# Kernel optimization log

Hardware: AMD Instinct MI355X
Metric: run time of the kernel (lower is better)

Reference implementation:

```python
import jax, jax.numpy as jnp
import numpy as np

N_NODES = 50000
N_EDGES = 300000
N_GRAPHS = 256
F_IN = 78
H1 = 10
F_H1 = 78
F_OUT = 128
NEG_SLOPE = 0.2  # PyG GATConv default leaky_relu slope


def gat_conv(x, src, dst, W, a_src, a_dst, bias, heads, out_dim):
    """PyG GATConv (eval mode): linear -> per-edge attention -> segment softmax over
    destination nodes -> scatter-add aggregation -> concat heads + bias.
    src/dst already include self-loops."""
    N = x.shape[0]
    h = (x @ W).reshape(N, heads, out_dim)              # [N,H,F]
    al_s = (h * a_src[None]).sum(-1)                     # [N,H]
    al_d = (h * a_dst[None]).sum(-1)                     # [N,H]
    e = jax.nn.leaky_relu(al_s[src] + al_d[dst], NEG_SLOPE)  # [E,H]
    m = jax.ops.segment_max(e, dst, num_segments=N)      # stable softmax per dst node
    w = jnp.exp(e - m[dst])
    denom = jax.ops.segment_sum(w, dst, num_segments=N)
    alpha = w / denom[dst]                               # [E,H]
    out = jax.ops.segment_sum(h[src] * alpha[:, :, None], dst, num_segments=N)
    return out.reshape(N, heads * out_dim) + bias


def setup_inputs() -> dict:
    key = jax.random.key(0)
    ks = jax.random.split(key, 16)
    x = jax.random.normal(ks[0], (N_NODES, F_IN), dtype=jnp.float32)
    edge_index = jax.random.randint(ks[1], (2, N_EDGES), 0, N_NODES, dtype=jnp.int32)
    batch = jnp.sort(jax.random.randint(ks[2], (N_NODES,), 0, N_GRAPHS, dtype=jnp.int32))
    s = 0.1
    W1 = jax.random.normal(ks[3], (F_IN, H1 * F_H1), dtype=jnp.float32) * s
    a_src1 = jax.random.normal(ks[4], (H1, F_H1), dtype=jnp.float32) * s
    a_dst1 = jax.random.normal(ks[5], (H1, F_H1), dtype=jnp.float32) * s
    b1 = jnp.zeros((H1 * F_H1,), dtype=jnp.float32)
    W2 = jax.random.normal(ks[6], (H1 * F_H1, F_OUT), dtype=jnp.float32) * s
    a_src2 = jax.random.normal(ks[7], (1, F_OUT), dtype=jnp.float32) * s
    a_dst2 = jax.random.normal(ks[8], (1, F_OUT), dtype=jnp.float32) * s
    b2 = jnp.zeros((F_OUT,), dtype=jnp.float32)
    fc_w = jax.random.normal(ks[9], (F_OUT, F_OUT), dtype=jnp.float32) * s
    fc_b = jnp.zeros((F_OUT,), dtype=jnp.float32)
    return dict(x=x, edge_index=edge_index, batch=batch, W1=W1, a_src1=a_src1,
                a_dst1=a_dst1, b1=b1, W2=W2, a_src2=a_src2, a_dst2=a_dst2, b2=b2,
                fc_w=fc_w, fc_b=fc_b)


def reference(x, edge_index, batch, W1, a_src1, a_dst1, b1, W2, a_src2, a_dst2, b2, fc_w, fc_b):
    N = x.shape[0]
    loop = jnp.arange(N, dtype=edge_index.dtype)
    src = jnp.concatenate([edge_index[0], loop])  # add self-loops (PyG default)
    dst = jnp.concatenate([edge_index[1], loop])
    # dropout layers are identity in eval mode
    h = jax.nn.elu(gat_conv(x, src, dst, W1, a_src1, a_dst1, b1, H1, F_H1))
    h = gat_conv(h, src, dst, W2, a_src2, a_dst2, b2, 1, F_OUT)
    h = jax.nn.relu(h)
    g = jax.ops.segment_max(h, batch, num_segments=N_GRAPHS)  # global max pool [B,F]
    out = jax.nn.relu(g @ fc_w + fc_b)
    return out
```

## Files before the change

### kernel.cpp

```cpp
#include <hip/hip_runtime.h>
#include <hip/hip_bf16.h>

#define N_NODES 50000
#define N_EDGES 300000
#define E_TOT   350000
#define N_GRAPHS 256
#define F_IN 78
#define H1 10
#define D1 780
#define F_OUT 128
#define KP 800
#define K1P 96
#define NEG_SLOPE 0.2f
#define NB 196

typedef float v4f __attribute__((ext_vector_type(4)));
typedef short v8s __attribute__((ext_vector_type(8)));

__device__ __forceinline__ int src_of(int e, const int* __restrict__ ei) {
  return (e < N_EDGES) ? ei[e] : (e - N_EDGES);
}
__device__ __forceinline__ int dst_of(int e, const int* __restrict__ ei) {
  return (e < N_EDGES) ? ei[N_EDGES + e] : (e - N_EDGES);
}


__global__ void k_deg(const int* __restrict__ ei, int* __restrict__ deg) {
  int e = blockIdx.x * 256 + threadIdx.x;
  if (e >= E_TOT) return;
  atomicAdd(&deg[dst_of(e, ei)], 1);
}

__global__ void k_scan1(const int* __restrict__ deg, int* __restrict__ part) {
  __shared__ int s[256];
  int t = threadIdx.x;
  int i = blockIdx.x * 256 + t;
  s[t] = (i < N_NODES) ? deg[i] : 0;
  __syncthreads();
  for (int d = 128; d > 0; d >>= 1) {
    if (t < d) s[t] += s[t + d];
    __syncthreads();
  }
  if (t == 0) part[blockIdx.x] = s[0];
}

__global__ void k_scan2(const int* __restrict__ part, int* __restrict__ ppref) {
  if (threadIdx.x == 0) {
    int run = 0;
    for (int i = 0; i < NB; ++i) { ppref[i] = run; run += part[i]; }
  }
}

__global__ void k_scan3(const int* __restrict__ deg, const int* __restrict__ ppref,
                        int* __restrict__ offs, int* __restrict__ cursor) {
  __shared__ int s[256];
  int t = threadIdx.x;
  int i = blockIdx.x * 256 + t;
  int v = (i < N_NODES) ? deg[i] : 0;
  s[t] = v;
  __syncthreads();
  for (int d = 1; d < 256; d <<= 1) {
    int u = (t >= d) ? s[t - d] : 0;
    __syncthreads();
    s[t] += u;
    __syncthreads();
  }
  int excl = s[t] - v;
  if (i < N_NODES) {
    int off = ppref[blockIdx.x] + excl;
    offs[i] = off;
    cursor[i] = off;
  }
}

__global__ void k_scatter(const int* __restrict__ ei, int* __restrict__ cursor,
                          int* __restrict__ src_s, int* __restrict__ dst_s) {
  int e = blockIdx.x * 256 + threadIdx.x;
  if (e >= E_TOT) return;
  int s = src_of(e, ei);
  int d = dst_of(e, ei);
  int pos = atomicAdd(&cursor[d], 1);
  src_s[pos] = s;
  dst_s[pos] = d;
}


__global__ void k_prep(const float* __restrict__ W1, const float* __restrict__ as1,
                       const float* __restrict__ ad1, float* __restrict__ was,
                       float* __restrict__ wad) {
  int i = blockIdx.x * 256 + threadIdx.x;
  if (i >= F_IN * H1) return;
  int k = i / H1, h = i - k * H1;
  const float* wrow = W1 + (size_t)k * D1 + h * 78;
  const float* ar = as1 + h * 78;
  const float* br = ad1 + h * 78;
  float s = 0.f, d = 0.f;
  for (int f = 0; f < 78; ++f) {
    float w = wrow[f];
    s = fmaf(w, ar[f], s);
    d = fmaf(w, br[f], d);
  }
  was[i] = s;
  wad[i] = d;
}


__global__ __launch_bounds__(320) void k_logits1(const float* __restrict__ x,
                                                 const float* __restrict__ was,
                                                 const float* __restrict__ wad,
                                                 float* __restrict__ als,
                                                 float* __restrict__ ald) {
  __shared__ float xs[32][81];
  __shared__ float wl[D1], wl2[D1];
  int tid = threadIdx.x;
  int n0 = blockIdx.x * 32;
  for (int i = tid; i < 32 * F_IN; i += 320) {
    int r = i / F_IN, k = i - r * F_IN;
    int n = n0 + r;
    xs[r][k] = (n < N_NODES) ? x[(size_t)n * F_IN + k] : 0.f;
  }
  for (int i = tid; i < D1; i += 320) { wl[i] = was[i]; wl2[i] = wad[i]; }
  __syncthreads();
  int r = tid / 10, h = tid - r * 10;
  int n = n0 + r;
  float s = 0.f, d = 0.f;
  for (int k = 0; k < F_IN; ++k) {
    float xv = xs[r][k];
    s = fmaf(xv, wl[k * 10 + h], s);
    d = fmaf(xv, wl2[k * 10 + h], d);
  }
  if (n < N_NODES) { als[n * 10 + h] = s; ald[n * 10 + h] = d; }
}


__global__ void k_w1e(const float* __restrict__ als1, const float* __restrict__ ald1,
                      const int* __restrict__ src_s, const int* __restrict__ dst_s,
                      float* __restrict__ w1) {
  int i = blockIdx.x * 256 + threadIdx.x;
  if (i >= E_TOT * H1) return;
  int pos = i / H1, h = i - pos * H1;
  float v = als1[src_s[pos] * H1 + h] + ald1[dst_s[pos] * H1 + h];
  v = (v > 0.f) ? v : NEG_SLOPE * v;
  w1[i] = __expf(v);
}


__global__ void k_w1t(const float* __restrict__ W1, __hip_bfloat16* __restrict__ T) {
  int i = blockIdx.x * 256 + threadIdx.x;
  if (i >= 800 * K1P) return;
  int r = i / K1P, k = i - r * K1P;
  float v = (r < D1 && k < F_IN) ? W1[(size_t)k * D1 + r] : 0.f;
  T[i] = __float2bfloat16(v);
}


__global__ void k_w2t(const float* __restrict__ W2, __hip_bfloat16* __restrict__ Bt) {
  int i = blockIdx.x * 256 + threadIdx.x;
  if (i >= F_OUT * KP) return;
  int c = i / KP, k = i - c * KP;
  float v = (k < D1) ? W2[(size_t)k * F_OUT + c] : 0.f;
  Bt[i] = __float2bfloat16(v);
}


__global__ __launch_bounds__(512, 4) void k_l12(const float* __restrict__ x,
                                                const float* __restrict__ w1,
                                                const int* __restrict__ src_s,
                                                const int* __restrict__ offs,
                                                const int* __restrict__ deg,
                                                const __hip_bfloat16* __restrict__ W1T,
                                                const float* __restrict__ b1,
                                                const __hip_bfloat16* __restrict__ W2T,
                                                const float* __restrict__ a_src2,
                                                const float* __restrict__ a_dst2,
                                                float* __restrict__ h2,
                                                float* __restrict__ als2,
                                                float* __restrict__ ald2) {
  __shared__ __align__(16) unsigned char lds[33792];
  __hip_bfloat16* xbb = (__hip_bfloat16*)lds;
  __hip_bfloat16* out1t = (__hip_bfloat16*)lds;
  float* h2t = (float*)(lds + 25600);
#define XB(h, g, k) xbb[((h) * 16 + (g)) * 104 + (k)]

  int tid = threadIdx.x, wid = tid >> 6, lane = tid & 63;
  int n0 = blockIdx.x * 16;
  int col16 = lane & 15, kq = (lane >> 4) * 8;

  {
    unsigned int* p = (unsigned int*)lds;
    for (int i = tid; i < H1 * 16 * 52; i += 512) p[i] = 0u;
  }
  __syncthreads();

  #pragma unroll
  for (int rep = 0; rep < 2; ++rep) {
    int g = wid * 2 + rep;
    int n = n0 + g;
    int o = __builtin_amdgcn_readfirstlane(offs[n]);
    int d = __builtin_amdgcn_readfirstlane(deg[n]);
    float acc[H1], acc2[H1];
    #pragma unroll
    for (int h = 0; h < H1; ++h) { acc[h] = 0.f; acc2[h] = 0.f; }

    float onesel = (lane == 14) ? 1.0f : 0.f;
    int j = 0;
    for (; j + 4 <= d; j += 4) {
      int e0 = o + j;
      int s0 = src_s[e0], s1 = src_s[e0 + 1], s2 = src_s[e0 + 2], s3 = src_s[e0 + 3];
      const float* x0 = x + (size_t)s0 * F_IN;
      const float* x1 = x + (size_t)s1 * F_IN;
      const float* x2 = x + (size_t)s2 * F_IN;
      const float* x3 = x + (size_t)s3 * F_IN;
      float xa0 = x0[lane], xa1 = x1[lane], xa2 = x2[lane], xa3 = x3[lane];
      float xb0 = (lane < 14) ? x0[64 + lane] : onesel;
      float xb1 = (lane < 14) ? x1[64 + lane] : onesel;
      float xb2 = (lane < 14) ? x2[64 + lane] : onesel;
      float xb3 = (lane < 14) ? x3[64 + lane] : onesel;
      const float* wp = w1 + (size_t)e0 * H1;
      #pragma unroll
      for (int h = 0; h < H1; ++h) {
        float wa = wp[h], wb = wp[10 + h], wc = wp[20 + h], wd = wp[30 + h];
        acc[h] = fmaf(wa, xa0, acc[h]);
        acc[h] = fmaf(wb, xa1, acc[h]);
        acc[h] = fmaf(wc, xa2, acc[h]);
        acc[h] = fmaf(wd, xa3, acc[h]);
        acc2[h] = fmaf(wa, xb0, acc2[h]);
        acc2[h] = fmaf(wb, xb1, acc2[h]);
        acc2[h] = fmaf(wc, xb2, acc2[h]);
        acc2[h] = fmaf(wd, xb3, acc2[h]);
      }
    }
    for (; j < d; ++j) {
      int e0 = o + j;
      int s0 = src_s[e0];
      const float* x0 = x + (size_t)s0 * F_IN;
      float xa0 = x0[lane];
      float xb0 = (lane < 14) ? x0[64 + lane] : onesel;
      const float* wp = w1 + (size_t)e0 * H1;
      #pragma unroll
      for (int h = 0; h < H1; ++h) {
        float wa = wp[h];
        acc[h] = fmaf(wa, xa0, acc[h]);
        acc2[h] = fmaf(wa, xb0, acc2[h]);
      }
    }
    #pragma unroll
    for (int h = 0; h < H1; ++h) {
      float inv = 1.f / __shfl(acc2[h], 14);
      XB(h, g, lane) = __float2bfloat16(acc[h] * inv);
      if (lane < 14) XB(h, g, 64 + lane) = __float2bfloat16(acc2[h] * inv);
    }
  }
  __syncthreads();

  const unsigned short* Bp1 = (const unsigned short*)W1T;
  v4f res[7];
  int nu = 0;
  for (int u = wid; u < 50; u += 8) {
    int h = u / 5, nt = u - (u / 5) * 5;
    v4f acc = (v4f){0.f, 0.f, 0.f, 0.f};
    #pragma unroll
    for (int kt = 0; kt < 3; ++kt) {
      v8s a = *reinterpret_cast<const v8s*>(&XB(h, col16, kt * 32 + kq));
      v8s b = *reinterpret_cast<const v8s*>(
          &Bp1[(size_t)(h * 78 + nt * 16 + col16) * K1P + kt * 32 + kq]);
      acc = __builtin_amdgcn_mfma_f32_16x16x32_bf16(a, b, acc, 0, 0, 0);
    }
    res[nu++] = acc;
  }
  __syncthreads();

  if (tid < 160) {
    int node = tid / 10, cc = (tid - node * 10) * 2;
    *(unsigned int*)&out1t[node * 800 + 780 + cc] = 0u;
  }
  nu = 0;
  for (int u = wid; u < 50; u += 8) {
    int h = u / 5, nt = u - (u / 5) * 5;
    v4f acc = res[nu++];
    int cl = nt * 16 + col16;
    if (cl < 78) {
      int c = h * 78 + cl;
      float bv = b1[c];
      #pragma unroll
      for (int r = 0; r < 4; ++r) {
        int node = (lane >> 4) * 4 + r;
        float v = acc[r] + bv;
        v = (v > 0.f) ? v : expm1f(v);
        out1t[node * 800 + c] = __float2bfloat16(v);
      }
    }
  }
  __syncthreads();

  const unsigned short* Bp2 = (const unsigned short*)W2T;
  v4f acc3 = (v4f){0.f, 0.f, 0.f, 0.f};
  #pragma unroll 5
  for (int kt = 0; kt < 25; ++kt) {
    int k = kt * 32 + kq;
    v8s a = *reinterpret_cast<const v8s*>(&out1t[col16 * 800 + k]);
    v8s b = *reinterpret_cast<const v8s*>(&Bp2[(size_t)(wid * 16 + col16) * KP + k]);
    acc3 = __builtin_amdgcn_mfma_f32_16x16x32_bf16(a, b, acc3, 0, 0, 0);
  }
  {
    int col = wid * 16 + col16;
    #pragma unroll
    for (int r = 0; r < 4; ++r) {
      int node = (lane >> 4) * 4 + r;
      h2[(size_t)(n0 + node) * F_OUT + col] = acc3[r];
      h2t[node * F_OUT + col] = acc3[r];
    }
  }
  __syncthreads();

  #pragma unroll
  for (int rep = 0; rep < 2; ++rep) {
    int nn = wid * 2 + rep;
    float v0 = h2t[nn * F_OUT + lane], v1 = h2t[nn * F_OUT + 64 + lane];
    float s = v0 * a_src2[lane] + v1 * a_src2[64 + lane];
    float dd = v0 * a_dst2[lane] + v1 * a_dst2[64 + lane];
    #pragma unroll
    for (int off = 32; off > 0; off >>= 1) {
      s += __shfl_down(s, off);
      dd += __shfl_down(dd, off);
    }
    if (lane == 0) { als2[n0 + nn] = s; ald2[n0 + nn] = dd; }
  }
#undef XB
}


__global__ __launch_bounds__(512) void k_agg2f(const float* __restrict__ h2,
                                               const float* __restrict__ als2,
                                               const float* __restrict__ ald2,
                                               const int* __restrict__ src_s,
                                               const int* __restrict__ offs,
                                               const int* __restrict__ deg,
                                               const float* __restrict__ b2,
                                               const int* __restrict__ batch,
                                               unsigned int* __restrict__ g) {
  int tid = threadIdx.x;
  int n = blockIdx.x * 4 + (tid >> 7);
  int f = tid & 127;
  int o = __builtin_amdgcn_readfirstlane(offs[n]);
  int d = __builtin_amdgcn_readfirstlane(deg[n]);
  float aldn = ald2[n];
  float acc = 0.f, ssum = 0.f;
  int j = 0;
  for (; j + 4 <= d; j += 4) {
    float wq[4], hq[4];
    #pragma unroll
    for (int q = 0; q < 4; ++q) {
      int e = o + j + q;
      int sb = src_s[e];
      float v = als2[sb] + aldn;
      v = (v > 0.f) ? v : NEG_SLOPE * v;
      wq[q] = __expf(v);
      hq[q] = h2[(size_t)sb * F_OUT + f];
    }
    #pragma unroll
    for (int q = 0; q < 4; ++q) {
      ssum += wq[q];
      acc = fmaf(wq[q], hq[q], acc);
    }
  }
  for (; j < d; ++j) {
    int e = o + j;
    int sb = src_s[e];
    float v = als2[sb] + aldn;
    v = (v > 0.f) ? v : NEG_SLOPE * v;
    float w = __expf(v);
    ssum += w;
    acc = fmaf(w, h2[(size_t)sb * F_OUT + f], acc);
  }
  float v = fmaxf(acc / ssum + b2[f], 0.f);
  int gc = __builtin_amdgcn_readfirstlane(batch[n]);
  atomicMax(&g[gc * F_OUT + f], __float_as_uint(v));
}


__global__ __launch_bounds__(128) void k_fc(const float* __restrict__ g,
                                            const float* __restrict__ fc_w,
                                            const float* __restrict__ fc_b,
                                            float* __restrict__ out) {
  int b = blockIdx.x, c = threadIdx.x;
  const float* gr = g + (size_t)b * F_OUT;
  float acc = 0.f;
  for (int k = 0; k < F_OUT; ++k) acc = fmaf(gr[k], fc_w[k * F_OUT + c], acc);
  float v = acc + fc_b[c];
  out[(size_t)b * F_OUT + c] = fmaxf(v, 0.f);
}


extern "C" void kernel_launch(void* const* d_in, const int* in_sizes, int n_in,
                              void* d_out, int out_size, void* d_ws, size_t ws_size,
                              hipStream_t stream) {
  const float* x      = (const float*)d_in[0];
  const int*   ei     = (const int*)  d_in[1];
  const int*   batch  = (const int*)  d_in[2];
  const float* W1     = (const float*)d_in[3];
  const float* a_src1 = (const float*)d_in[4];
  const float* a_dst1 = (const float*)d_in[5];
  const float* b1     = (const float*)d_in[6];
  const float* W2     = (const float*)d_in[7];
  const float* a_src2 = (const float*)d_in[8];
  const float* a_dst2 = (const float*)d_in[9];
  const float* b2     = (const float*)d_in[10];
  const float* fc_w   = (const float*)d_in[11];
  const float* fc_b   = (const float*)d_in[12];
  float* out = (float*)d_out;

  float* ws = (float*)d_ws;
  float* h2   = ws;
  float* als1 = ws + 6400000;
  float* ald1 = ws + 6900000;
  float* als2 = ws + 7400000;
  float* ald2 = ws + 7450000;
  float* g    = ws + 7500000;
  float* was  = ws + 7533000;
  float* wad  = ws + 7534000;
  __hip_bfloat16* W2T = (__hip_bfloat16*)(ws + 7535000);
  __hip_bfloat16* W1T = (__hip_bfloat16*)(ws + 7587000);
  float* w1   = ws + 7626000;
  int* ib     = (int*)(ws + 11126000);
  int* deg    = ib;
  int* offs   = ib + 50000;
  int* cursor = ib + 100000;
  int* src_s  = ib + 150000;
  int* dst_s  = ib + 500000;
  int* part   = ib + 850000;
  int* ppref  = ib + 850224;

  hipMemsetAsync(deg, 0, N_NODES * sizeof(int), stream);
  k_deg<<<(E_TOT + 255) / 256, 256, 0, stream>>>(ei, deg);
  k_scan1<<<NB, 256, 0, stream>>>(deg, part);
  k_scan2<<<1, 64, 0, stream>>>(part, ppref);
  k_scan3<<<NB, 256, 0, stream>>>(deg, ppref, offs, cursor);
  k_scatter<<<(E_TOT + 255) / 256, 256, 0, stream>>>(ei, cursor, src_s, dst_s);

  k_prep<<<4, 256, 0, stream>>>(W1, a_src1, a_dst1, was, wad);
  k_w1t<<<(800 * K1P + 255) / 256, 256, 0, stream>>>(W1, W1T);
  k_w2t<<<(F_OUT * KP + 255) / 256, 256, 0, stream>>>(W2, W2T);
  hipMemsetAsync(g, 0, N_GRAPHS * F_OUT * sizeof(float), stream);

  k_logits1<<<(N_NODES + 31) / 32, 320, 0, stream>>>(x, was, wad, als1, ald1);
  k_w1e<<<(E_TOT * H1 + 255) / 256, 256, 0, stream>>>(als1, ald1, src_s, dst_s, w1);

  k_l12<<<N_NODES / 16, 512, 0, stream>>>(x, w1, src_s, offs, deg, W1T, b1,
                                          W2T, a_src2, a_dst2, h2, als2, ald2);

  k_agg2f<<<(N_NODES + 3) / 4, 512, 0, stream>>>(h2, als2, ald2, src_s, offs, deg,
                                                 b2, batch, (unsigned int*)g);

  k_fc<<<N_GRAPHS, F_OUT, 0, stream>>>(g, fc_w, fc_b, out);
}
```

Before: 267.1 us.

## Sort nodes by degree to balance per-wave work in aggregation kernels

Adds a counting sort of nodes by in-degree (histogram, scan, scatter kernels) and makes the fused layer kernel and the layer-2 aggregation process nodes in that order through an indirection array. Waves in a block then handle nodes of similar degree, which is meant to reduce divergence and idle time from uneven neighbour counts. In exchange it adds three small kernels, an extra indirection load, scattered writes of h2 and logits, and less locality in reads of per-node data.

```diff
diff --git a/kernel.cpp b/kernel.cpp
--- a/kernel.cpp
+++ b/kernel.cpp
@@ -82,6 +82,28 @@
   int pos = atomicAdd(&cursor[d], 1);
   src_s[pos] = s;
   dst_s[pos] = d;
+}
+
+
+__global__ void k_dhist(const int* __restrict__ deg, int* __restrict__ hist) {
+  int n = blockIdx.x * 256 + threadIdx.x;
+  if (n >= N_NODES) return;
+  atomicAdd(&hist[min(deg[n], 63)], 1);
+}
+
+__global__ void k_dscan(const int* __restrict__ hist, int* __restrict__ bincur) {
+  if (threadIdx.x == 0) {
+    int run = 0;
+    for (int i = 0; i < 64; ++i) { bincur[i] = run; run += hist[i]; }
+  }
+}
+
+__global__ void k_dscatter(const int* __restrict__ deg, int* __restrict__ bincur,
+                           int* __restrict__ nsort) {
+  int n = blockIdx.x * 256 + threadIdx.x;
+  if (n >= N_NODES) return;
+  int pos = atomicAdd(&bincur[min(deg[n], 63)], 1);
+  nsort[pos] = n;
 }
 
 
@@ -168,6 +190,7 @@
                                                 const int* __restrict__ src_s,
                                                 const int* __restrict__ offs,
                                                 const int* __restrict__ deg,
+                                                const int* __restrict__ nsort,
                                                 const __hip_bfloat16* __restrict__ W1T,
                                                 const float* __restrict__ b1,
                                                 const __hip_bfloat16* __restrict__ W2T,
@@ -177,6 +200,7 @@
                                                 float* __restrict__ als2,
                                                 float* __restrict__ ald2) {
   __shared__ __align__(16) unsigned char lds[33792];
+  __shared__ int nid[16];
   __hip_bfloat16* xbb = (__hip_bfloat16*)lds;
   __hip_bfloat16* out1t = (__hip_bfloat16*)lds;
   float* h2t = (float*)(lds + 25600);
@@ -186,6 +210,7 @@
   int n0 = blockIdx.x * 16;
   int col16 = lane & 15, kq = (lane >> 4) * 8;
 
+  if (tid < 16) nid[tid] = nsort[n0 + tid];
   {
     unsigned int* p = (unsigned int*)lds;
     for (int i = tid; i < H1 * 16 * 52; i += 512) p[i] = 0u;
@@ -195,7 +220,7 @@
   #pragma unroll
   for (int rep = 0; rep < 2; ++rep) {
     int g = wid * 2 + rep;
-    int n = n0 + g;
+    int n = nid[g];
     int o = __builtin_amdgcn_readfirstlane(offs[n]);
     int d = __builtin_amdgcn_readfirstlane(deg[n]);
     float acc[H1], acc2[H1];
@@ -307,7 +332,7 @@
     #pragma unroll
     for (int r = 0; r < 4; ++r) {
       int node = (lane >> 4) * 4 + r;
-      h2[(size_t)(n0 + node) * F_OUT + col] = acc3[r];
+      h2[(size_t)nid[node] * F_OUT + col] = acc3[r];
       h2t[node * F_OUT + col] = acc3[r];
     }
   }
@@ -324,7 +349,7 @@
       s += __shfl_down(s, off);
       dd += __shfl_down(dd, off);
     }
-    if (lane == 0) { als2[n0 + nn] = s; ald2[n0 + nn] = dd; }
+    if (lane == 0) { als2[nid[nn]] = s; ald2[nid[nn]] = dd; }
   }
 #undef XB
 }
@@ -336,11 +361,12 @@
                                                const int* __restrict__ src_s,
                                                const int* __restrict__ offs,
                                                const int* __restrict__ deg,
+                                               const int* __restrict__ nsort,
                                                const float* __restrict__ b2,
                                                const int* __restrict__ batch,
                                                unsigned int* __restrict__ g) {
   int tid = threadIdx.x;
-  int n = blockIdx.x * 4 + (tid >> 7);
+  int n = nsort[blockIdx.x * 4 + (tid >> 7)];
   int f = tid & 127;
   int o = __builtin_amdgcn_readfirstlane(offs[n]);
   int d = __builtin_amdgcn_readfirstlane(deg[n]);
@@ -430,13 +456,20 @@
   int* dst_s  = ib + 500000;
   int* part   = ib + 850000;
   int* ppref  = ib + 850224;
+  int* hist   = ib + 850448;
+  int* bincur = ib + 850512;
+  int* nsort  = ib + 850576;
 
   hipMemsetAsync(deg, 0, N_NODES * sizeof(int), stream);
+  hipMemsetAsync(hist, 0, 64 * sizeof(int), stream);
   k_deg<<<(E_TOT + 255) / 256, 256, 0, stream>>>(ei, deg);
   k_scan1<<<NB, 256, 0, stream>>>(deg, part);
   k_scan2<<<1, 64, 0, stream>>>(part, ppref);
   k_scan3<<<NB, 256, 0, stream>>>(deg, ppref, offs, cursor);
   k_scatter<<<(E_TOT + 255) / 256, 256, 0, stream>>>(ei, cursor, src_s, dst_s);
+  k_dhist<<<NB, 256, 0, stream>>>(deg, hist);
+  k_dscan<<<1, 64, 0, stream>>>(hist, bincur);
+  k_dscatter<<<NB, 256, 0, stream>>>(deg, bincur, nsort);
 
   k_prep<<<4, 256, 0, stream>>>(W1, a_src1, a_dst1, was, wad);
   k_w1t<<<(800 * K1P + 255) / 256, 256, 0, stream>>>(W1, W1T);
@@ -446,11 +479,11 @@
   k_logits1<<<(N_NODES + 31) / 32, 320, 0, stream>>>(x, was, wad, als1, ald1);
   k_w1e<<<(E_TOT * H1 + 255) / 256, 256, 0, stream>>>(als1, ald1, src_s, dst_s, w1);
 
-  k_l12<<<N_NODES / 16, 512, 0, stream>>>(x, w1, src_s, offs, deg, W1T, b1,
+  k_l12<<<N_NODES / 16, 512, 0, stream>>>(x, w1, src_s, offs, deg, nsort, W1T, b1,
                                           W2T, a_src2, a_dst2, h2, als2, ald2);
 
   k_agg2f<<<(N_NODES + 3) / 4, 512, 0, stream>>>(h2, als2, ald2, src_s, offs, deg,
-                                                 b2, batch, (unsigned int*)g);
+                                                 nsort, b2, batch, (unsigned int*)g);
 
   k_fc<<<N_GRAPHS, F_OUT, 0, stream>>>(g, fc_w, fc_b, out);
 }
```

Result: slower. 641.2 us (+140.0%).

## Pad per-node CSR segments to multiples of eight to drop remainder loop

Applied to the files above, without the earlier changes.

Each node's incoming-edge segment in the sorted CSR is padded to a multiple of 8, with padding entries marked by dst=-1, src=0 and given zero attention weight. The layer-1 aggregation loop then processes 8 edges per iteration with no scalar tail, giving more independent gathers in flight. The cost is roughly doubled edge storage, two extra memsets, and a larger k_w1e launch that touches padded slots. Padded edges still gather row 0 of x and spend FMAs on zero weights, and other kernels that read offs/deg, such as k_agg2f, must agree with the new padded offsets.

```diff
diff --git a/kernel.cpp b/kernel.cpp
--- a/kernel.cpp
+++ b/kernel.cpp
@@ -4,6 +4,7 @@
 #define N_NODES 50000
 #define N_EDGES 300000
 #define E_TOT   350000
+#define EPAD_MAX 700000
 #define N_GRAPHS 256
 #define F_IN 78
 #define H1 10
@@ -35,7 +36,7 @@
   __shared__ int s[256];
   int t = threadIdx.x;
   int i = blockIdx.x * 256 + t;
-  s[t] = (i < N_NODES) ? deg[i] : 0;
+  s[t] = (i < N_NODES) ? ((deg[i] + 7) & ~7) : 0;
   __syncthreads();
   for (int d = 128; d > 0; d >>= 1) {
     if (t < d) s[t] += s[t + d];
@@ -56,7 +57,7 @@
   __shared__ int s[256];
   int t = threadIdx.x;
   int i = blockIdx.x * 256 + t;
-  int v = (i < N_NODES) ? deg[i] : 0;
+  int v = (i < N_NODES) ? ((deg[i] + 7) & ~7) : 0;
   s[t] = v;
   __syncthreads();
   for (int d = 1; d < 256; d <<= 1) {
@@ -137,11 +138,16 @@
                       const int* __restrict__ src_s, const int* __restrict__ dst_s,
                       float* __restrict__ w1) {
   int i = blockIdx.x * 256 + threadIdx.x;
-  if (i >= E_TOT * H1) return;
+  if (i >= EPAD_MAX * H1) return;
   int pos = i / H1, h = i - pos * H1;
-  float v = als1[src_s[pos] * H1 + h] + ald1[dst_s[pos] * H1 + h];
-  v = (v > 0.f) ? v : NEG_SLOPE * v;
-  w1[i] = __expf(v);
+  int dn = dst_s[pos];
+  float w = 0.f;
+  if (dn >= 0) {
+    float v = als1[src_s[pos] * H1 + h] + ald1[dn * H1 + h];
+    v = (v > 0.f) ? v : NEG_SLOPE * v;
+    w = __expf(v);
+  }
+  w1[i] = w;
 }
 
 
@@ -198,50 +204,33 @@
     int n = n0 + g;
     int o = __builtin_amdgcn_readfirstlane(offs[n]);
     int d = __builtin_amdgcn_readfirstlane(deg[n]);
+    int dp = (d + 7) & ~7;
     float acc[H1], acc2[H1];
     #pragma unroll
     for (int h = 0; h < H1; ++h) { acc[h] = 0.f; acc2[h] = 0.f; }
 
     float onesel = (lane == 14) ? 1.0f : 0.f;
-    int j = 0;
-    for (; j + 4 <= d; j += 4) {
+    for (int j = 0; j < dp; j += 8) {
       int e0 = o + j;
-      int s0 = src_s[e0], s1 = src_s[e0 + 1], s2 = src_s[e0 + 2], s3 = src_s[e0 + 3];
-      const float* x0 = x + (size_t)s0 * F_IN;
-      const float* x1 = x + (size_t)s1 * F_IN;
-      const float* x2 = x + (size_t)s2 * F_IN;
-      const float* x3 = x + (size_t)s3 * F_IN;
-      float xa0 = x0[lane], xa1 = x1[lane], xa2 = x2[lane], xa3 = x3[lane];
-      float xb0 = (lane < 14) ? x0[64 + lane] : onesel;
-      float xb1 = (lane < 14) ? x1[64 + lane] : onesel;
-      float xb2 = (lane < 14) ? x2[64 + lane] : onesel;
-      float xb3 = (lane < 14) ? x3[64 + lane] : onesel;
+      int ss[8];
+      #pragma unroll
+      for (int q = 0; q < 8; ++q) ss[q] = src_s[e0 + q];
+      float xa[8], xb[8];
+      #pragma unroll
+      for (int q = 0; q < 8; ++q) {
+        const float* xr = x + (size_t)ss[q] * F_IN;
+        xa[q] = xr[lane];
+        xb[q] = (lane < 14) ? xr[64 + lane] : onesel;
+      }
       const float* wp = w1 + (size_t)e0 * H1;
       #pragma unroll
       for (int h = 0; h < H1; ++h) {
-        float wa = wp[h], wb = wp[10 + h], wc = wp[20 + h], wd = wp[30 + h];
-        acc[h] = fmaf(wa, xa0, acc[h]);
-        acc[h] = fmaf(wb, xa1, acc[h]);
-        acc[h] = fmaf(wc, xa2, acc[h]);
-        acc[h] = fmaf(wd, xa3, acc[h]);
-        acc2[h] = fmaf(wa, xb0, acc2[h]);
-        acc2[h] = fmaf(wb, xb1, acc2[h]);
-        acc2[h] = fmaf(wc, xb2, acc2[h]);
-        acc2[h] = fmaf(wd, xb3, acc2[h]);
-      }
-    }
-    for (; j < d; ++j) {
-      int e0 = o + j;
-      int s0 = src_s[e0];
-      const float* x0 = x + (size_t)s0 * F_IN;
-      float xa0 = x0[lane];
-      float xb0 = (lane < 14) ? x0[64 + lane] : onesel;
-      const float* wp = w1 + (size_t)e0 * H1;
-      #pragma unroll
-      for (int h = 0; h < H1; ++h) {
-        float wa = wp[h];
-        acc[h] = fmaf(wa, xa0, acc[h]);
-        acc2[h] = fmaf(wa, xb0, acc2[h]);
+        #pragma unroll
+        for (int q = 0; q < 8; ++q) {
+          float w = wp[q * 10 + h];
+          acc[h] = fmaf(w, xa[q], acc[h]);
+          acc2[h] = fmaf(w, xb[q], acc2[h]);
+        }
       }
     }
     #pragma unroll
@@ -422,16 +411,18 @@
   __hip_bfloat16* W2T = (__hip_bfloat16*)(ws + 7535000);
   __hip_bfloat16* W1T = (__hip_bfloat16*)(ws + 7587000);
   float* w1   = ws + 7626000;
-  int* ib     = (int*)(ws + 11126000);
+  int* ib     = (int*)(ws + 14626000);
   int* deg    = ib;
   int* offs   = ib + 50000;
   int* cursor = ib + 100000;
   int* src_s  = ib + 150000;
-  int* dst_s  = ib + 500000;
-  int* part   = ib + 850000;
-  int* ppref  = ib + 850224;
+  int* dst_s  = ib + 850000;
+  int* part   = ib + 1550000;
+  int* ppref  = ib + 1550224;
 
   hipMemsetAsync(deg, 0, N_NODES * sizeof(int), stream);
+  hipMemsetAsync(src_s, 0, EPAD_MAX * sizeof(int), stream);
+  hipMemsetAsync(dst_s, 0xFF, EPAD_MAX * sizeof(int), stream);
   k_deg<<<(E_TOT + 255) / 256, 256, 0, stream>>>(ei, deg);
   k_scan1<<<NB, 256, 0, stream>>>(deg, part);
   k_scan2<<<1, 64, 0, stream>>>(part, ppref);
@@ -444,7 +435,7 @@
   hipMemsetAsync(g, 0, N_GRAPHS * F_OUT * sizeof(float), stream);
 
   k_logits1<<<(N_NODES + 31) / 32, 320, 0, stream>>>(x, was, wad, als1, ald1);
-  k_w1e<<<(E_TOT * H1 + 255) / 256, 256, 0, stream>>>(als1, ald1, src_s, dst_s, w1);
+  k_w1e<<<(EPAD_MAX * H1 + 255) / 256, 256, 0, stream>>>(als1, ald1, src_s, dst_s, w1);
 
   k_l12<<<N_NODES / 16, 512, 0, stream>>>(x, w1, src_s, offs, deg, W1T, b1,
                                           W2T, a_src2, a_dst2, h2, als2, ald2);
```

Result: slower. 279.2 us, median of 6 (+4.5%).
